# Optimization experiments

Hardware: AMD Instinct MI355X
Metric: run time of the kernel (lower is better)

## Reference

```python
import jax, jax.numpy as jnp
from jax import lax
import numpy as np

# ---- module hyperparameters (from init_kwargs) ----
DIM = 256
DIM_HEAD = 64
HEADS = 4
GROUPS = 4                      # offset_groups (defaults to heads)
INNER = DIM_HEAD * HEADS        # 256
OFF_DIMS = INNER // GROUPS      # 64
DOWN = 4
KS = 6
PAD = (KS - DOWN) // 2          # 1
OFFSET_SCALE = float(DOWN)      # offset_scale defaults to down_sample_factor
CPB_DIM = DIM // 4              # 64
SCALE = DIM_HEAD ** -0.5


def make_grid(h, w, dtype):
    # torch.meshgrid(arange(w), arange(h), indexing='xy') stacked at dim 0:
    # channel 0 = x (column index), channel 1 = y (row index); shape [2,h,w]
    yy, xx = jnp.meshgrid(jnp.arange(h), jnp.arange(w), indexing='ij')
    return jnp.stack([xx, yy], axis=0).astype(dtype)


def normalize_grid_c(vg):
    # vg: [..., 2, h, w] -> [..., h, w, 2]; faithful to source: channel 0
    # normalized by (h-1), channel 1 by (w-1) (source's h/w naming quirk).
    h, w = vg.shape[-2:]
    gh = 2.0 * vg[..., 0, :, :] / max(h - 1, 1) - 1.0
    gw = 2.0 * vg[..., 1, :, :] / max(w - 1, 1) - 1.0
    return jnp.stack([gh, gw], axis=-1)


def grid_sample_zeros(img, grid):
    # F.grid_sample bilinear, padding_mode='zeros', align_corners=False
    # img: [N,C,H,W]; grid: [N,Hg,Wg,2] with (..,0)=x, (..,1)=y in [-1,1]
    N, C, H, W = img.shape
    ix = ((grid[..., 0] + 1.0) * W - 1.0) * 0.5
    iy = ((grid[..., 1] + 1.0) * H - 1.0) * 0.5
    x0 = jnp.floor(ix)
    y0 = jnp.floor(iy)

    def gather(yy, xx):
        valid = (xx >= 0) & (xx <= W - 1) & (yy >= 0) & (yy <= H - 1)
        xc = jnp.clip(xx, 0, W - 1).astype(jnp.int32)
        yc = jnp.clip(yy, 0, H - 1).astype(jnp.int32)
        vals = jax.vmap(lambda im, y_, x_: im[:, y_, x_])(img, yc, xc)  # [N,C,Hg,Wg]
        return vals * valid[:, None, :, :].astype(img.dtype)

    wa = (x0 + 1 - ix) * (y0 + 1 - iy)
    wb = (ix - x0) * (y0 + 1 - iy)
    wc = (x0 + 1 - ix) * (iy - y0)
    wd = (ix - x0) * (iy - y0)
    return (gather(y0, x0) * wa[:, None]
            + gather(y0, x0 + 1) * wb[:, None]
            + gather(y0 + 1, x0) * wc[:, None]
            + gather(y0 + 1, x0 + 1) * wd[:, None])


def gconv1x1(t, w):
    # grouped 1x1 conv (no bias): t [b, G*Ci, h, w], w [G, Co, Ci]
    G, Co, Ci = w.shape
    bb, _, hh, ww = t.shape
    tg = t.reshape(bb, G, Ci, hh, ww)
    return jnp.einsum('bgihw,goi->bgohw', tg, w).reshape(bb, G * Co, hh, ww)


def setup_inputs() -> dict:
    key = jax.random.key(0)
    ks = jax.random.split(key, 12)
    s = 0.02
    B, H, W = 8, 32, 32
    cg = DIM // GROUPS  # per-group in-channels = 64
    og = INNER // GROUPS  # per-group out-channels = 64
    return {
        'x': jax.random.normal(ks[0], (B, DIM, H, W), jnp.float32),
        'wq': jax.random.normal(ks[1], (GROUPS, og, cg), jnp.float32) * s,
        'wk': jax.random.normal(ks[2], (GROUPS, og, cg), jnp.float32) * s,
        'wv': jax.random.normal(ks[3], (GROUPS, og, cg), jnp.float32) * s,
        'w_off_dw': jax.random.normal(ks[4], (OFF_DIMS, 1, KS, KS), jnp.float32) * s,
        'b_off_dw': jnp.zeros((OFF_DIMS,), jnp.float32),
        'w_off_pw': jax.random.normal(ks[5], (2, OFF_DIMS), jnp.float32) * s,
        'cpb_w1': jax.random.normal(ks[6], (CPB_DIM, 2), jnp.float32) * s,
        'cpb_b1': jnp.zeros((CPB_DIM,), jnp.float32),
        'cpb_w2': jax.random.normal(ks[7], (CPB_DIM, CPB_DIM), jnp.float32) * s,
        'cpb_b2': jnp.zeros((CPB_DIM,), jnp.float32),
        'cpb_w3': jax.random.normal(ks[8], (HEADS // GROUPS, CPB_DIM), jnp.float32) * s,
        'cpb_b3': jnp.zeros((HEADS // GROUPS,), jnp.float32),
        'w_out': jax.random.normal(ks[9], (DIM, INNER), jnp.float32) * s,
        'b_out': jnp.zeros((DIM,), jnp.float32),
    }


def reference(x, wq, wk, wv, w_off_dw, b_off_dw, w_off_pw,
              cpb_w1, cpb_b1, cpb_w2, cpb_b2, cpb_w3, cpb_b3,
              w_out, b_out):
    b, _, H, W = x.shape

    q = gconv1x1(x, wq)                                       # [b, INNER, H, W]
    gq = q.reshape(b * GROUPS, OFF_DIMS, H, W)                # grouped queries
    gx = x.reshape(b * GROUPS, DIM // GROUPS, H, W)           # grouped input

    # to_offsets: depthwise conv -> GELU -> 1x1 conv -> tanh -> scale
    off = lax.conv_general_dilated(
        gq, w_off_dw, window_strides=(DOWN, DOWN),
        padding=[(PAD, PAD), (PAD, PAD)],
        dimension_numbers=('NCHW', 'OIHW', 'NCHW'),
        feature_group_count=OFF_DIMS)
    off = off + b_off_dw[None, :, None, None]
    off = jax.nn.gelu(off, approximate=False)
    off = jnp.einsum('bchw,oc->bohw', off, w_off_pw)
    off = jnp.tanh(off) * OFFSET_SCALE                        # [bg, 2, h2, w2]

    h2, w2 = off.shape[-2:]
    vg = make_grid(h2, w2, off.dtype)[None] + off             # [bg, 2, h2, w2]
    vgs = normalize_grid_c(vg)                                # [bg, h2, w2, 2]

    kv = grid_sample_zeros(gx, vgs)                           # [bg, DIM/G, h2, w2]
    kv = kv.reshape(b, DIM, h2, w2)
    k = gconv1x1(kv, wk)
    v = gconv1x1(kv, wv)
    q = q * SCALE

    def to_heads(t):
        bb, _, hh, ww = t.shape
        return t.reshape(bb, HEADS, DIM_HEAD, hh * ww).transpose(0, 1, 3, 2)

    qh, kh, vh = to_heads(q), to_heads(k), to_heads(v)        # [b, h, i|j, d]
    sim = jnp.einsum('bhid,bhjd->bhij', qh, kh)               # [b, h, HW, h2*w2]

    # CPB relative position bias
    grid_q = normalize_grid_c(make_grid(H, W, x.dtype)).reshape(1, H * W, 2)
    grid_kv = vgs.reshape(b * GROUPS, h2 * w2, 2)
    pos = grid_q[:, :, None, :] - grid_kv[:, None, :, :]      # [bg, i, j, 2]
    bias = jnp.sign(pos) * jnp.log1p(jnp.abs(pos))
    bias = jax.nn.relu(bias @ cpb_w1.T + cpb_b1)
    bias = jax.nn.relu(bias @ cpb_w2.T + cpb_b2)
    bias = bias @ cpb_w3.T + cpb_b3                           # [bg, i, j, o]
    o = HEADS // GROUPS
    bias = bias.reshape(b, GROUPS, H * W, h2 * w2, o)
    bias = bias.transpose(0, 1, 4, 2, 3).reshape(b, HEADS, H * W, h2 * w2)

    attn = jax.nn.softmax(sim + bias, axis=-1)
    out = jnp.einsum('bhij,bhjd->bhid', attn, vh)             # [b, h, HW, d]
    out = out.transpose(0, 1, 3, 2).reshape(b, INNER, H, W)
    out = jnp.einsum('bchw,oc->bohw', out, w_out) + b_out[None, :, None, None]
    return out
```

## Files before the change

kernel.cpp:

```cpp
#include <hip/hip_runtime.h>
#include <hip/hip_bf16.h>
#include <math.h>

#define QSCALE 0.125f

typedef __attribute__((ext_vector_type(8))) short short8b;
typedef __attribute__((ext_vector_type(8))) _Float16 half8;
typedef __attribute__((ext_vector_type(2))) _Float16 half2v;
typedef __attribute__((ext_vector_type(4))) float f32x4;

__device__ __forceinline__ uint pack2(float a, float b) {
    uint r;
    asm("v_cvt_pk_bf16_f32 %0, %1, %2" : "=v"(r) : "v"(a), "v"(b));
    return r;
}
__device__ __forceinline__ uint pkrtz(float a, float b) {
    uint r;
    asm("v_cvt_pkrtz_f16_f32 %0, %1, %2" : "=v"(r) : "v"(a), "v"(b));
    return r;
}
__device__ __forceinline__ half2v h2(uint u) { return __builtin_bit_cast(half2v, u); }
__device__ __forceinline__ float slogf_(float p) {
    return copysignf(log1pf(fabsf(p)), p);
}

__global__ __launch_bounds__(256) void k_qproj(const float* __restrict__ x,
                                               const float* __restrict__ wq,
                                               float* __restrict__ q,
                                               short* __restrict__ qbt) {
    __shared__ uint wqh[64 * 36];
    __shared__ uint xsT[128 * 36];
    int ht = blockIdx.x, g = blockIdx.y, b = blockIdx.z;
    int tid = threadIdx.x;
    for (int e = tid; e < 2048; e += 256) {
        int co = e >> 5, p = e & 31;
        float2 w2v = *(const float2*)&wq[(g * 64 + co) * 64 + 2 * p];
        wqh[co * 36 + p] = pkrtz(w2v.x, w2v.y);
    }
    const float* xb = x + (b * 256 + g * 64) * 1024 + ht * 128;
    for (int e = tid; e < 4096; e += 256) {
        int p = e >> 7, hw = e & 127;
        float lo = xb[(2 * p) * 1024 + hw];
        float hi = xb[(2 * p + 1) * 1024 + hw];
        xsT[hw * 36 + p] = pkrtz(lo, hi);
    }
    __syncthreads();
    int wid = tid >> 6, lane = tid & 63, lr = lane & 15, g4 = lane >> 4;
    half8 af[4][2];
    #pragma unroll
    for (int m = 0; m < 4; m++)
        #pragma unroll
        for (int s = 0; s < 2; s++)
            af[m][s] = __builtin_bit_cast(half8,
                *(const uint4*)&wqh[(m * 16 + lr) * 36 + s * 16 + g4 * 4]);
    f32x4 acc[4][2];
    #pragma unroll
    for (int m = 0; m < 4; m++)
        #pragma unroll
        for (int nt = 0; nt < 2; nt++) acc[m][nt] = (f32x4){0.f, 0.f, 0.f, 0.f};
    #pragma unroll
    for (int s = 0; s < 2; s++)
        #pragma unroll
        for (int nt = 0; nt < 2; nt++) {
            half8 bf = __builtin_bit_cast(half8,
                *(const uint4*)&xsT[(wid * 32 + nt * 16 + lr) * 36 + s * 16 + g4 * 4]);
            #pragma unroll
            for (int m = 0; m < 4; m++)
                acc[m][nt] = __builtin_amdgcn_mfma_f32_16x16x32_f16(af[m][s], bf, acc[m][nt], 0, 0, 0);
        }
    float* qb = q + (b * 256 + g * 64) * 1024 + ht * 128;
    #pragma unroll
    for (int m = 0; m < 4; m++)
        #pragma unroll
        for (int nt = 0; nt < 2; nt++) {
            int hw = wid * 32 + nt * 16 + lr;
            #pragma unroll
            for (int r = 0; r < 4; r++)
                qb[(m * 16 + g4 * 4 + r) * 1024 + hw] = acc[m][nt][r];
        }
    short* q16 = qbt + ((size_t)((b * 4 + g) * 1024 + ht * 128)) * 64;
    #pragma unroll
    for (int nt = 0; nt < 2; nt++) {
        int hw = wid * 32 + nt * 16 + lr;
        #pragma unroll
        for (int m = 0; m < 4; m++) {
            uint2 uu;
            uu.x = pack2(acc[m][nt][0] * QSCALE, acc[m][nt][1] * QSCALE);
            uu.y = pack2(acc[m][nt][2] * QSCALE, acc[m][nt][3] * QSCALE);
            *(uint2*)&q16[hw * 64 + m * 16 + g4 * 4] = uu;
        }
    }
}

__global__ __launch_bounds__(256) void k_dw(const float* __restrict__ q,
                                            const float* __restrict__ wdw,
                                            const float* __restrict__ bdw,
                                            float* __restrict__ gdw) {
    __shared__ float qs[8 * 1024];
    __shared__ float wds[8 * 36];
    int cg = blockIdx.x, n = blockIdx.y;
    int b = n >> 2, gg = n & 3;
    int c0 = cg * 8;
    int tid = threadIdx.x;
    const float* qn = q + (b * 256 + gg * 64 + c0) * 1024;
    for (int e = tid; e < 2048; e += 256)
        ((float4*)qs)[e] = ((const float4*)qn)[e];
    for (int e = tid; e < 288; e += 256)
        wds[e] = wdw[c0 * 36 + e];
    __syncthreads();
    for (int e = tid; e < 512; e += 256) {
        int c = e >> 6, pos = e & 63;
        int oy = pos >> 3, ox = pos & 7;
        float acc = bdw[c0 + c];
        #pragma unroll
        for (int ky = 0; ky < 6; ky++) {
            int iy = oy * 4 - 1 + ky;
            if (iy < 0 || iy > 31) continue;
            #pragma unroll
            for (int kx = 0; kx < 6; kx++) {
                int ix = ox * 4 - 1 + kx;
                if (ix < 0 || ix > 31) continue;
                acc += qs[c * 1024 + iy * 32 + ix] * wds[c * 36 + ky * 6 + kx];
            }
        }
        gdw[(n * 64 + c0 + c) * 64 + pos] = acc * 0.5f * (1.f + erff(acc * 0.70710678118654752f));
    }
}

__global__ __launch_bounds__(256) void k_pre(const float* __restrict__ x,
                                             const float* __restrict__ gdw,
                                             const float* __restrict__ wpw,
                                             const float* __restrict__ wk,
                                             const float* __restrict__ wv,
                                             const float* __restrict__ wout,
                                             const float* __restrict__ w2,
                                             float* __restrict__ vgs,
                                             uint* __restrict__ u0g,
                                             short* __restrict__ kob,
                                             short* __restrict__ vob,
                                             short* __restrict__ wob,
                                             uint* __restrict__ w2h) {
    __shared__ float gstage[4096];
    __shared__ float kvsT[64 * 68];
    __shared__ uint wkh[64 * 36];
    __shared__ uint wvh[64 * 36];
    __shared__ uint kvh[64 * 36];
    __shared__ float vx_s[64], vy_s[64];
    int n = blockIdx.x, tid = threadIdx.x;
    int b = n >> 2, g = n & 3;

    {
        int e = n * 2048 + tid * 8;
        float4 f0 = *(const float4*)&wout[e];
        float4 f1 = *(const float4*)&wout[e + 4];
        uint4 u = {pack2(f0.x, f0.y), pack2(f0.z, f0.w), pack2(f1.x, f1.y), pack2(f1.z, f1.w)};
        *(uint4*)&wob[e] = u;
    }
    if (tid < 128) {
        int idx = n * 128 + tid;
        int c2 = idx >> 5, p = idx & 31;
        float2 wv2 = *(const float2*)&w2[c2 * 64 + 2 * p];
        w2h[c2 * 32 + p] = pkrtz(wv2.x, wv2.y);
    }
    for (int e = tid; e < 2048; e += 256) {
        int co = e >> 5, p = e & 31;
        float2 a = *(const float2*)&wk[(g * 64 + co) * 64 + 2 * p];
        float2 c = *(const float2*)&wv[(g * 64 + co) * 64 + 2 * p];
        wkh[co * 36 + p] = pkrtz(a.x, a.y);
        wvh[co * 36 + p] = pkrtz(c.x, c.y);
    }
    for (int e = tid; e < 1024; e += 256)
        ((float4*)gstage)[e] = ((const float4*)(gdw + n * 4096))[e];
    __syncthreads();
    if (tid < 128) {
        int o = tid >> 6, pos = tid & 63;
        float a = 0.f;
        #pragma unroll 8
        for (int c = 0; c < 64; c++) a += gstage[c * 64 + pos] * wpw[o * 64 + c];
        float off = tanhf(a) * 4.0f;
        if (o == 0) {
            int ox = pos & 7;
            float v = 2.f * ((float)ox + off) / 7.f - 1.f;
            vx_s[pos] = v;
            vgs[(n * 64 + pos) * 2] = v;
        } else {
            int oy = pos >> 3;
            float v = 2.f * ((float)oy + off) / 7.f - 1.f;
            vy_s[pos] = v;
            vgs[(n * 64 + pos) * 2 + 1] = v;
        }
    }
    __syncthreads();
    for (int e = tid; e < 2048; e += 256) {
        int ix = e >> 6, j = e & 63;
        float qx = (2.f / 31.f) * (float)ix - 1.f;
        float u = slogf_(qx - vx_s[j]);
        u0g[n * 2048 + e] = pkrtz(u, u);
    }
    for (int e = tid; e < 4096; e += 256) {
        int c = e >> 6, pos = e & 63;
        float ix = (vx_s[pos] + 1.f) * 16.f - 0.5f;
        float iy = (vy_s[pos] + 1.f) * 16.f - 0.5f;
        float x0 = floorf(ix), y0 = floorf(iy);
        float wa = (x0 + 1.f - ix) * (y0 + 1.f - iy);
        float wb = (ix - x0) * (y0 + 1.f - iy);
        float wc = (x0 + 1.f - ix) * (iy - y0);
        float wd = (ix - x0) * (iy - y0);
        const float* img = x + (b * 256 + g * 64 + c) * 1024;
        int xi = (int)x0, yi = (int)y0;
        float acc = 0.f;
        if (xi >= 0 && xi <= 31 && yi >= 0 && yi <= 31)             acc += img[yi * 32 + xi] * wa;
        if (xi + 1 >= 0 && xi + 1 <= 31 && yi >= 0 && yi <= 31)     acc += img[yi * 32 + xi + 1] * wb;
        if (xi >= 0 && xi <= 31 && yi + 1 >= 0 && yi + 1 <= 31)     acc += img[(yi + 1) * 32 + xi] * wc;
        if (xi + 1 >= 0 && xi + 1 <= 31 && yi + 1 >= 0 && yi + 1 <= 31) acc += img[(yi + 1) * 32 + xi + 1] * wd;
        kvsT[pos * 68 + c] = acc;
    }
    __syncthreads();
    for (int e = tid; e < 2048; e += 256) {
        int pos = e >> 5, p = e & 31;
        float2 v2 = *(const float2*)&kvsT[pos * 68 + 2 * p];
        kvh[pos * 36 + p] = pkrtz(v2.x, v2.y);
    }
    __syncthreads();
    int wid = tid >> 6, lane = tid & 63, lr = lane & 15, gq = lane >> 4;
    int mat = wid >> 1, cb = (wid & 1) * 32;
    const uint* wh = mat ? wvh : wkh;
    #pragma unroll
    for (int ct2 = 0; ct2 < 2; ct2++) {
        int ct = cb + ct2 * 16;
        half8 af[2];
        #pragma unroll
        for (int s = 0; s < 2; s++)
            af[s] = __builtin_bit_cast(half8, *(const uint4*)&wh[(ct + lr) * 36 + s * 16 + gq * 4]);
        #pragma unroll
        for (int nt = 0; nt < 4; nt++) {
            half8 bf[2];
            #pragma unroll
            for (int s = 0; s < 2; s++)
                bf[s] = __builtin_bit_cast(half8, *(const uint4*)&kvh[(nt * 16 + lr) * 36 + s * 16 + gq * 4]);
            f32x4 acc = {0.f, 0.f, 0.f, 0.f};
            acc = __builtin_amdgcn_mfma_f32_16x16x32_f16(af[0], bf[0], acc, 0, 0, 0);
            acc = __builtin_amdgcn_mfma_f32_16x16x32_f16(af[1], bf[1], acc, 0, 0, 0);
            if (mat == 0) {
                uint2 uu = {pack2(acc[0], acc[1]), pack2(acc[2], acc[3])};
                *(uint2*)&kob[n * 4096 + (nt * 16 + lr) * 64 + ct + gq * 4] = uu;
            } else {
                #pragma unroll
                for (int r = 0; r < 4; r++)
                    vob[n * 4096 + (ct + gq * 4 + r) * 64 + nt * 16 + lr] = (short)pack2(acc[r], acc[r]);
            }
        }
    }
}

__global__ __launch_bounds__(256) void k_cpb(const float* __restrict__ vgs,
                                             const uint* __restrict__ u0g,
                                             const float* __restrict__ w1,
                                             const float* __restrict__ b1,
                                             const uint* __restrict__ w2h,
                                             const float* __restrict__ b2,
                                             const float* __restrict__ w3,
                                             const float* __restrict__ b3,
                                             const short* __restrict__ qbt,
                                             const short* __restrict__ kob,
                                             const short* __restrict__ vob,
                                             short* __restrict__ attb) {
    __shared__ uint Q1p[64 * 36];
    __shared__ uint u0p[32 * 64];
    __shared__ float u1t[64];
    __shared__ uint w1ps[32];
    __shared__ float w3s[64];
    __shared__ float b2s[64];
    __shared__ float biasS[32 * 68];
    int iy = blockIdx.x, n = blockIdx.y, tid = threadIdx.x;
    float qy = 2.f * (float)iy / 31.f - 1.f;

    if (tid < 64) u1t[tid] = slogf_(qy - vgs[(n << 7) + tid * 2 + 1]);
    if (tid >= 64 && tid < 96) {
        int p = tid - 64;
        int s = p >> 4, gg = (p >> 2) & 3, pp = p & 3;
        int k = s * 32 + gg * 8 + 2 * pp;
        w1ps[p] = pkrtz(w1[2 * k], w1[2 * k + 2]);
    }
    if (tid >= 128 && tid < 192) w3s[tid - 128] = w3[tid - 128];
    if (tid >= 192) b2s[tid - 192] = b2[tid - 192];
    __syncthreads();
    for (int e = tid; e < 2048; e += 256) {
        int j = e >> 5, pp = e & 31;
        int k = pp * 2;
        float lo = fmaf(w1[2 * k + 1], u1t[j], b1[k]);
        float hi = fmaf(w1[2 * k + 3], u1t[j], b1[k + 1]);
        Q1p[j * 36 + pp] = pkrtz(lo, hi);
    }
    for (int e = tid; e < 2048; e += 256)
        u0p[e] = u0g[n * 2048 + e];

    int wid = tid >> 6, lane = tid & 63, lr = lane & 15, g = lane >> 4;
    float b3v = b3[0];

    half8 w2f[4][2];
    #pragma unroll
    for (int m = 0; m < 4; m++)
        #pragma unroll
        for (int s = 0; s < 2; s++)
            w2f[m][s] = __builtin_bit_cast(half8,
                *(const uint4*)&w2h[(m * 16 + lr) * 32 + s * 16 + g * 4]);
    __syncthreads();

    const half2v hz = {(_Float16)0, (_Float16)0};
    for (int ii = 0; ii < 8; ii++) {
        int ixl = wid * 8 + ii;
        #pragma unroll
        for (int nt = 0; nt < 4; nt++) {
            half2v u0v = h2(u0p[ixl * 64 + nt * 16 + lr]);
            const uint* q1p = &Q1p[(nt * 16 + lr) * 36];
            half8 bfr[2];
            #pragma unroll
            for (int s = 0; s < 2; s++) {
                uint4 q4 = *(const uint4*)&q1p[s * 16 + g * 4];
                uint4 wp4 = *(const uint4*)&w1ps[s * 16 + g * 4];
                half2v h0 = __builtin_elementwise_max(h2(wp4.x) * u0v + h2(q4.x), hz);
                half2v h1v = __builtin_elementwise_max(h2(wp4.y) * u0v + h2(q4.y), hz);
                half2v h2v_ = __builtin_elementwise_max(h2(wp4.z) * u0v + h2(q4.z), hz);
                half2v h3 = __builtin_elementwise_max(h2(wp4.w) * u0v + h2(q4.w), hz);
                uint4 hb = {__builtin_bit_cast(uint, h0), __builtin_bit_cast(uint, h1v),
                            __builtin_bit_cast(uint, h2v_), __builtin_bit_cast(uint, h3)};
                bfr[s] = __builtin_bit_cast(half8, hb);
            }
            f32x4 acc[4];
            #pragma unroll
            for (int m = 0; m < 4; m++) {
                f32x4 cseed = *(const f32x4*)&b2s[m * 16 + g * 4];
                acc[m] = __builtin_amdgcn_mfma_f32_16x16x32_f16(w2f[m][0], bfr[0], cseed, 0, 0, 0);
            }
            #pragma unroll
            for (int m = 0; m < 4; m++)
                acc[m] = __builtin_amdgcn_mfma_f32_16x16x32_f16(w2f[m][1], bfr[1], acc[m], 0, 0, 0);
            f32x4 tv = {0.f, 0.f, 0.f, 0.f};
            #pragma unroll
            for (int m = 0; m < 4; m++) {
                f32x4 r = __builtin_elementwise_max(acc[m], (f32x4){0.f, 0.f, 0.f, 0.f});
                f32x4 w3m = *(const f32x4*)&w3s[m * 16 + g * 4];
                tv += w3m * r;
            }
            float t = (tv[0] + tv[1]) + (tv[2] + tv[3]);
            t += __shfl_xor(t, 16);
            t += __shfl_xor(t, 32);
            if (g == nt) biasS[ixl * 68 + lane] = t + b3v;
        }
    }
    __syncthreads();

    if (wid < 2) {
        int lb = wid * 16;
        float* P = &biasS[lb * 68];
        int i0w = iy * 32 + lb;
        const short* kb = kob + n * 4096;
        const short* vb = vob + n * 4096;
        const short* qb = qbt + ((size_t)n * 1024 + i0w + lr) * 64;
        short8b qf[2];
        qf[0] = *(const short8b*)&qb[g * 8];
        qf[1] = *(const short8b*)&qb[32 + g * 8];
        float bv[4][4];
        #pragma unroll
        for (int r = 0; r < 4; r++)
            #pragma unroll
            for (int nt = 0; nt < 4; nt++)
                bv[r][nt] = biasS[(lb + g * 4 + r) * 68 + nt * 16 + lr];

        f32x4 acc[4];
        #pragma unroll
        for (int nt = 0; nt < 4; nt++) {
            short8b kf0 = *(const short8b*)&kb[(nt * 16 + lr) * 64 + g * 8];
            short8b kf1 = *(const short8b*)&kb[(nt * 16 + lr) * 64 + 32 + g * 8];
            acc[nt] = (f32x4){0.f, 0.f, 0.f, 0.f};
            acc[nt] = __builtin_amdgcn_mfma_f32_16x16x32_bf16(qf[0], kf0, acc[nt], 0, 0, 0);
            acc[nt] = __builtin_amdgcn_mfma_f32_16x16x32_bf16(qf[1], kf1, acc[nt], 0, 0, 0);
        }
        #pragma unroll
        for (int r = 0; r < 4; r++) {
            float s0 = acc[0][r] + bv[r][0], s1 = acc[1][r] + bv[r][1];
            float s2 = acc[2][r] + bv[r][2], s3 = acc[3][r] + bv[r][3];
            float m = fmaxf(fmaxf(s0, s1), fmaxf(s2, s3));
            m = fmaxf(m, __shfl_xor(m, 1));
            m = fmaxf(m, __shfl_xor(m, 2));
            m = fmaxf(m, __shfl_xor(m, 4));
            m = fmaxf(m, __shfl_xor(m, 8));
            float e0 = __expf(s0 - m), e1 = __expf(s1 - m);
            float e2 = __expf(s2 - m), e3 = __expf(s3 - m);
            float sum = (e0 + e1) + (e2 + e3);
            sum += __shfl_xor(sum, 1);
            sum += __shfl_xor(sum, 2);
            sum += __shfl_xor(sum, 4);
            sum += __shfl_xor(sum, 8);
            float inv = 1.f / sum;
            int row = g * 4 + r;
            P[row * 68 + lr]      = e0 * inv;
            P[row * 68 + 16 + lr] = e1 * inv;
            P[row * 68 + 32 + lr] = e2 * inv;
            P[row * 68 + 48 + lr] = e3 * inv;
        }
        const float* pr = &P[lr * 68];
        float4 a0 = *(float4*)&pr[g * 8];
        float4 a1 = *(float4*)&pr[g * 8 + 4];
        float4 a2 = *(float4*)&pr[32 + g * 8];
        float4 a3 = *(float4*)&pr[32 + g * 8 + 4];
        uint4 up0 = {pack2(a0.x, a0.y), pack2(a0.z, a0.w), pack2(a1.x, a1.y), pack2(a1.z, a1.w)};
        uint4 up1 = {pack2(a2.x, a2.y), pack2(a2.z, a2.w), pack2(a3.x, a3.y), pack2(a3.z, a3.w)};
        short8b pf0 = __builtin_bit_cast(short8b, up0);
        short8b pf1 = __builtin_bit_cast(short8b, up1);

        f32x4 oacc[4];
        #pragma unroll
        for (int nt = 0; nt < 4; nt++) {
            short8b vf0 = *(const short8b*)&vb[(nt * 16 + lr) * 64 + g * 8];
            short8b vf1 = *(const short8b*)&vb[(nt * 16 + lr) * 64 + 32 + g * 8];
            oacc[nt] = (f32x4){0.f, 0.f, 0.f, 0.f};
            oacc[nt] = __builtin_amdgcn_mfma_f32_16x16x32_bf16(pf0, vf0, oacc[nt], 0, 0, 0);
            oacc[nt] = __builtin_amdgcn_mfma_f32_16x16x32_bf16(pf1, vf1, oacc[nt], 0, 0, 0);
        }
        #pragma unroll
        for (int nt = 0; nt < 4; nt++)
            #pragma unroll
            for (int r = 0; r < 4; r++)
                P[(nt * 16 + lr) * 17 + g * 4 + r] = oacc[nt][r];
        int il = lane >> 2, dq = lane & 3;
        uint ub[8];
        #pragma unroll
        for (int t = 0; t < 8; t++) {
            float lo = P[(dq * 16 + 2 * t) * 17 + il];
            float hi = P[(dq * 16 + 2 * t + 1) * 17 + il];
            ub[t] = pack2(lo, hi);
        }
        int b_ = n >> 2, h_ = n & 3;
        short* op = attb + ((size_t)(b_ * 1024 + i0w + il)) * 256 + h_ * 64 + dq * 16;
        uint4 s0v = {ub[0], ub[1], ub[2], ub[3]};
        uint4 s1v = {ub[4], ub[5], ub[6], ub[7]};
        ((uint4*)op)[0] = s0v;
        ((uint4*)op)[1] = s1v;
    }
}

__global__ __launch_bounds__(256) void k_outproj(const short* __restrict__ attb,
                                                 const short* __restrict__ wob,
                                                 const float* __restrict__ bout,
                                                 float* __restrict__ y) {
    int rt = blockIdx.x;
    int ct = blockIdx.y;
    int tid = threadIdx.x, wid = tid >> 6, lane = tid & 63, lr = lane & 15, g = lane >> 4;
    int wr = wid >> 1, wc = wid & 1;
    int b = rt >> 5;
    int hw0 = (rt & 31) * 32 + wr * 16;
    int cobase = ct * 128 + wc * 64;
    const short* arow = attb + ((size_t)(b * 1024) + hw0) * 256;
    const short* brow = wob + (size_t)cobase * 256;

    f32x4 acc[4];
    #pragma unroll
    for (int nn = 0; nn < 4; nn++) acc[nn] = (f32x4){0.f, 0.f, 0.f, 0.f};
    #pragma unroll
    for (int s = 0; s < 8; s++) {
        short8b af = *(const short8b*)&arow[lr * 256 + s * 32 + g * 8];
        #pragma unroll
        for (int nn = 0; nn < 4; nn++) {
            short8b bf = *(const short8b*)&brow[(nn * 16 + lr) * 256 + s * 32 + g * 8];
            acc[nn] = __builtin_amdgcn_mfma_f32_16x16x32_bf16(af, bf, acc[nn], 0, 0, 0);
        }
    }
    #pragma unroll
    for (int nn = 0; nn < 4; nn++) {
        int co = cobase + nn * 16 + lr;
        float bo = bout[co];
        float4 o = {acc[nn][0] + bo, acc[nn][1] + bo, acc[nn][2] + bo, acc[nn][3] + bo};
        *(float4*)&y[(size_t)b * 262144 + (size_t)co * 1024 + hw0 + g * 4] = o;
    }
}

extern "C" void kernel_launch(void* const* d_in, const int* in_sizes, int n_in,
                              void* d_out, int out_size, void* d_ws, size_t ws_size,
                              hipStream_t stream) {
    const float* x    = (const float*)d_in[0];
    const float* wq   = (const float*)d_in[1];
    const float* wk   = (const float*)d_in[2];
    const float* wv   = (const float*)d_in[3];
    const float* wdw  = (const float*)d_in[4];
    const float* bdw  = (const float*)d_in[5];
    const float* wpw  = (const float*)d_in[6];
    const float* cw1  = (const float*)d_in[7];
    const float* cb1  = (const float*)d_in[8];
    const float* cw2  = (const float*)d_in[9];
    const float* cb2  = (const float*)d_in[10];
    const float* cw3  = (const float*)d_in[11];
    const float* cb3  = (const float*)d_in[12];
    const float* wout = (const float*)d_in[13];
    const float* bout = (const float*)d_in[14];
    float* y  = (float*)d_out;
    float* ws = (float*)d_ws;

    float* q    = ws;
    short* attb = (short*)ws;
    float* vgs  = ws + 4325376;
    short* qbt  = (short*)(ws + 4329472);
    short* kob  = (short*)(ws + 5378048);
    short* vob  = (short*)(ws + 5443584);
    float* gdw  = ws + 5509120;
    short* wob  = (short*)(ws + 5640192);
    uint*  u0g  = (uint*)(ws + 5672960);
    uint*  w2h  = (uint*)(ws + 5738496);

    k_qproj  <<<dim3(8, 4, 8),  256, 0, stream>>>(x, wq, q, qbt);
    k_dw     <<<dim3(8, 32),    256, 0, stream>>>(q, wdw, bdw, gdw);
    k_pre    <<<32,             256, 0, stream>>>(x, gdw, wpw, wk, wv, wout, cw2,
                                                  vgs, u0g, kob, vob, wob, w2h);
    k_cpb    <<<dim3(32, 32),   256, 0, stream>>>(vgs, u0g, cw1, cb1, w2h, cb2, cw3, cb3,
                                                  qbt, kob, vob, attb);
    k_outproj<<<dim3(256, 2),   256, 0, stream>>>(attb, wob, bout, y);
}
```

Baseline: 95.65 us.

## Split k_pre across position tiles and move wout conversion into k_qproj

k_pre now launches 4x more blocks (128 instead of 32), each handling a 16-position tile of the 64 sampled keys. Each block computes offsets, bilinear samples, and a single MFMA tile for K/V over those positions, which spreads a latency-bound 32-block kernel over more CUs. The bf16 conversion of the output-projection weight moves into k_qproj, whose 256 blocks each convert a slice. The cost is that every block redundantly converts the full wk/wv into fp16 in shared memory.

```diff
diff --git a/kernel.cpp b/kernel.cpp
--- a/kernel.cpp
+++ b/kernel.cpp
@@ -26,12 +26,22 @@
 
 __global__ __launch_bounds__(256) void k_qproj(const float* __restrict__ x,
                                                const float* __restrict__ wq,
+                                               const float* __restrict__ wout,
                                                float* __restrict__ q,
-                                               short* __restrict__ qbt) {
+                                               short* __restrict__ qbt,
+                                               short* __restrict__ wob) {
     __shared__ uint wqh[64 * 36];
     __shared__ uint xsT[128 * 36];
     int ht = blockIdx.x, g = blockIdx.y, b = blockIdx.z;
     int tid = threadIdx.x;
+    {
+        int bid = (blockIdx.z * 4 + blockIdx.y) * 8 + blockIdx.x;
+        if (tid < 128) {
+            int idx = bid * 128 + tid;
+            float2 w = *(const float2*)&wout[idx * 2];
+            *(uint*)&wob[idx * 2] = pack2(w.x, w.y);
+        }
+    }
     for (int e = tid; e < 2048; e += 256) {
         int co = e >> 5, p = e & 31;
         float2 w2v = *(const float2*)&wq[(g * 64 + co) * 64 + 2 * p];
@@ -132,32 +142,24 @@
                                              const float* __restrict__ wpw,
                                              const float* __restrict__ wk,
                                              const float* __restrict__ wv,
-                                             const float* __restrict__ wout,
                                              const float* __restrict__ w2,
                                              float* __restrict__ vgs,
                                              uint* __restrict__ u0g,
                                              short* __restrict__ kob,
                                              short* __restrict__ vob,
-                                             short* __restrict__ wob,
                                              uint* __restrict__ w2h) {
-    __shared__ float gstage[4096];
-    __shared__ float kvsT[64 * 68];
+    __shared__ float gq[64 * 16];
+    __shared__ float kvsT[16 * 68];
     __shared__ uint wkh[64 * 36];
     __shared__ uint wvh[64 * 36];
-    __shared__ uint kvh[64 * 36];
-    __shared__ float vx_s[64], vy_s[64];
-    int n = blockIdx.x, tid = threadIdx.x;
+    __shared__ uint kvh[16 * 36];
+    __shared__ float vx_s[16], vy_s[16];
+    int qt = blockIdx.x, n = blockIdx.y, tid = threadIdx.x;
     int b = n >> 2, g = n & 3;
-
-    {
-        int e = n * 2048 + tid * 8;
-        float4 f0 = *(const float4*)&wout[e];
-        float4 f1 = *(const float4*)&wout[e + 4];
-        uint4 u = {pack2(f0.x, f0.y), pack2(f0.z, f0.w), pack2(f1.x, f1.y), pack2(f1.z, f1.w)};
-        *(uint4*)&wob[e] = u;
-    }
-    if (tid < 128) {
-        int idx = n * 128 + tid;
+    int p0 = qt * 16;
+
+    if (qt == 0 && tid < 64) {
+        int idx = n * 64 + tid;
         int c2 = idx >> 5, p = idx & 31;
         float2 wv2 = *(const float2*)&w2[c2 * 64 + 2 * p];
         w2h[c2 * 32 + p] = pkrtz(wv2.x, wv2.y);
@@ -169,38 +171,41 @@
         wkh[co * 36 + p] = pkrtz(a.x, a.y);
         wvh[co * 36 + p] = pkrtz(c.x, c.y);
     }
-    for (int e = tid; e < 1024; e += 256)
-        ((float4*)gstage)[e] = ((const float4*)(gdw + n * 4096))[e];
-    __syncthreads();
-    if (tid < 128) {
-        int o = tid >> 6, pos = tid & 63;
+    for (int e = tid; e < 1024; e += 256) {
+        int c = e >> 4, p = e & 15;
+        gq[c * 16 + p] = gdw[n * 4096 + c * 64 + p0 + p];
+    }
+    __syncthreads();
+    if (tid < 32) {
+        int o = tid >> 4, p = tid & 15;
         float a = 0.f;
         #pragma unroll 8
-        for (int c = 0; c < 64; c++) a += gstage[c * 64 + pos] * wpw[o * 64 + c];
+        for (int c = 0; c < 64; c++) a += gq[c * 16 + p] * wpw[o * 64 + c];
         float off = tanhf(a) * 4.0f;
+        int pos = p0 + p;
         if (o == 0) {
             int ox = pos & 7;
             float v = 2.f * ((float)ox + off) / 7.f - 1.f;
-            vx_s[pos] = v;
+            vx_s[p] = v;
             vgs[(n * 64 + pos) * 2] = v;
         } else {
             int oy = pos >> 3;
             float v = 2.f * ((float)oy + off) / 7.f - 1.f;
-            vy_s[pos] = v;
+            vy_s[p] = v;
             vgs[(n * 64 + pos) * 2 + 1] = v;
         }
     }
     __syncthreads();
-    for (int e = tid; e < 2048; e += 256) {
-        int ix = e >> 6, j = e & 63;
+    for (int e = tid; e < 512; e += 256) {
+        int ix = e >> 4, j = e & 15;
         float qx = (2.f / 31.f) * (float)ix - 1.f;
         float u = slogf_(qx - vx_s[j]);
-        u0g[n * 2048 + e] = pkrtz(u, u);
-    }
-    for (int e = tid; e < 4096; e += 256) {
-        int c = e >> 6, pos = e & 63;
-        float ix = (vx_s[pos] + 1.f) * 16.f - 0.5f;
-        float iy = (vy_s[pos] + 1.f) * 16.f - 0.5f;
+        u0g[n * 2048 + ix * 64 + p0 + j] = pkrtz(u, u);
+    }
+    for (int e = tid; e < 1024; e += 256) {
+        int c = e >> 4, p = e & 15;
+        float ix = (vx_s[p] + 1.f) * 16.f - 0.5f;
+        float iy = (vy_s[p] + 1.f) * 16.f - 0.5f;
         float x0 = floorf(ix), y0 = floorf(iy);
         float wa = (x0 + 1.f - ix) * (y0 + 1.f - iy);
         float wb = (ix - x0) * (y0 + 1.f - iy);
@@ -213,42 +218,39 @@
         if (xi + 1 >= 0 && xi + 1 <= 31 && yi >= 0 && yi <= 31)     acc += img[yi * 32 + xi + 1] * wb;
         if (xi >= 0 && xi <= 31 && yi + 1 >= 0 && yi + 1 <= 31)     acc += img[(yi + 1) * 32 + xi] * wc;
         if (xi + 1 >= 0 && xi + 1 <= 31 && yi + 1 >= 0 && yi + 1 <= 31) acc += img[(yi + 1) * 32 + xi + 1] * wd;
-        kvsT[pos * 68 + c] = acc;
-    }
-    __syncthreads();
-    for (int e = tid; e < 2048; e += 256) {
-        int pos = e >> 5, p = e & 31;
-        float2 v2 = *(const float2*)&kvsT[pos * 68 + 2 * p];
-        kvh[pos * 36 + p] = pkrtz(v2.x, v2.y);
-    }
-    __syncthreads();
-    int wid = tid >> 6, lane = tid & 63, lr = lane & 15, gq = lane >> 4;
+        kvsT[p * 68 + c] = acc;
+    }
+    __syncthreads();
+    for (int e = tid; e < 512; e += 256) {
+        int p = e >> 5, pp = e & 31;
+        float2 v2 = *(const float2*)&kvsT[p * 68 + 2 * pp];
+        kvh[p * 36 + pp] = pkrtz(v2.x, v2.y);
+    }
+    __syncthreads();
+    int wid = tid >> 6, lane = tid & 63, lr = lane & 15, gq4 = lane >> 4;
     int mat = wid >> 1, cb = (wid & 1) * 32;
     const uint* wh = mat ? wvh : wkh;
+    half8 bf[2];
+    #pragma unroll
+    for (int s = 0; s < 2; s++)
+        bf[s] = __builtin_bit_cast(half8, *(const uint4*)&kvh[lr * 36 + s * 16 + gq4 * 4]);
     #pragma unroll
     for (int ct2 = 0; ct2 < 2; ct2++) {
         int ct = cb + ct2 * 16;
         half8 af[2];
         #pragma unroll
         for (int s = 0; s < 2; s++)
-            af[s] = __builtin_bit_cast(half8, *(const uint4*)&wh[(ct + lr) * 36 + s * 16 + gq * 4]);
-        #pragma unroll
-        for (int nt = 0; nt < 4; nt++) {
-            half8 bf[2];
-            #pragma unroll
-            for (int s = 0; s < 2; s++)
-                bf[s] = __builtin_bit_cast(half8, *(const uint4*)&kvh[(nt * 16 + lr) * 36 + s * 16 + gq * 4]);
-            f32x4 acc = {0.f, 0.f, 0.f, 0.f};
-            acc = __builtin_amdgcn_mfma_f32_16x16x32_f16(af[0], bf[0], acc, 0, 0, 0);
-            acc = __builtin_amdgcn_mfma_f32_16x16x32_f16(af[1], bf[1], acc, 0, 0, 0);
-            if (mat == 0) {
-                uint2 uu = {pack2(acc[0], acc[1]), pack2(acc[2], acc[3])};
-                *(uint2*)&kob[n * 4096 + (nt * 16 + lr) * 64 + ct + gq * 4] = uu;
-            } else {
-                #pragma unroll
-                for (int r = 0; r < 4; r++)
-                    vob[n * 4096 + (ct + gq * 4 + r) * 64 + nt * 16 + lr] = (short)pack2(acc[r], acc[r]);
-            }
+            af[s] = __builtin_bit_cast(half8, *(const uint4*)&wh[(ct + lr) * 36 + s * 16 + gq4 * 4]);
+        f32x4 acc = {0.f, 0.f, 0.f, 0.f};
+        acc = __builtin_amdgcn_mfma_f32_16x16x32_f16(af[0], bf[0], acc, 0, 0, 0);
+        acc = __builtin_amdgcn_mfma_f32_16x16x32_f16(af[1], bf[1], acc, 0, 0, 0);
+        if (mat == 0) {
+            uint2 uu = {pack2(acc[0], acc[1]), pack2(acc[2], acc[3])};
+            *(uint2*)&kob[n * 4096 + (p0 + lr) * 64 + ct + gq4 * 4] = uu;
+        } else {
+            #pragma unroll
+            for (int r = 0; r < 4; r++)
+                vob[n * 4096 + (ct + gq4 * 4 + r) * 64 + p0 + lr] = (short)pack2(acc[r], acc[r]);
         }
     }
 }
@@ -508,10 +510,10 @@
     uint*  u0g  = (uint*)(ws + 5672960);
     uint*  w2h  = (uint*)(ws + 5738496);
 
-    k_qproj  <<<dim3(8, 4, 8),  256, 0, stream>>>(x, wq, q, qbt);
+    k_qproj  <<<dim3(8, 4, 8),  256, 0, stream>>>(x, wq, wout, q, qbt, wob);
     k_dw     <<<dim3(8, 32),    256, 0, stream>>>(q, wdw, bdw, gdw);
-    k_pre    <<<32,             256, 0, stream>>>(x, gdw, wpw, wk, wv, wout, cw2,
-                                                  vgs, u0g, kob, vob, wob, w2h);
+    k_pre    <<<dim3(4, 32),    256, 0, stream>>>(x, gdw, wpw, wk, wv, cw2,
+                                                  vgs, u0g, kob, vob, w2h);
     k_cpb    <<<dim3(32, 32),   256, 0, stream>>>(vgs, u0g, cw1, cb1, w2h, cb2, cw3, cb3,
                                                   qbt, kob, vob, attb);
     k_outproj<<<dim3(256, 2),   256, 0, stream>>>(attb, wob, bout, y);
```

New measurement: 83.60 us. 1.14x faster.
